# Kernel optimization log

Measured on AMD Instinct MI355X. Metric: run time of the kernel, lower is better.

## Reference

```python
import jax, jax.numpy as jnp
import numpy as np

N = 16384      # number of points
DIM = 128      # feature dim
POS_DIM = 3
K = 16         # neighbors (init kwarg k)
SCALE = np.float32(np.sqrt(DIM))


def setup_inputs() -> dict:
    key = jax.random.key(0)
    ks = jax.random.split(key, 16)
    g = lambda i, shape: (jax.random.normal(ks[i], shape, dtype=jnp.float32) * 0.05)
    return {
        "x": jax.random.normal(ks[0], (N, DIM), dtype=jnp.float32),
        "pos": jax.random.uniform(ks[1], (N, POS_DIM), dtype=jnp.float32),
        # weights stored as (in, out); torch Linear applies x @ W.T + b
        "Wq": g(2, (DIM, DIM)),
        "Wk": g(3, (DIM, DIM)),
        "Wv": g(4, (DIM, DIM)),
        "mid_w1": g(5, (DIM, DIM)), "mid_b1": g(6, (DIM,)),
        "mid_w2": g(7, (DIM, DIM)), "mid_b2": g(8, (DIM,)),
        "pe_w1": g(9, (POS_DIM, DIM)), "pe_b1": g(10, (DIM,)),
        "pe_w2": g(11, (DIM, DIM)), "pe_b2": g(12, (DIM,)),
        "fin_w": g(13, (DIM, DIM)), "fin_b": g(14, (DIM,)),
    }


def _knn_indices(pos):
    # squared pairwise distances [N, N]; top-K smallest -> neighbor indices [N, K]
    sq = jnp.sum(pos * pos, axis=-1)
    d2 = sq[:, None] + sq[None, :] - 2.0 * (pos @ pos.T)
    _, ind = jax.lax.top_k(-d2, K)
    return ind


def reference(x, pos, Wq, Wk, Wv, mid_w1, mid_b1, mid_w2, mid_b2,
              pe_w1, pe_b1, pe_w2, pe_b2, fin_w, fin_b):
    ind = _knn_indices(pos)                    # [N, K] int32 (constant wrt grads)
    x_k = x[ind]                               # [N, K, D]
    pos_k = pos[ind]                           # [N, K, 3]
    rel = pos[:, None, :] - pos_k              # [N, K, 3]
    pe = jax.nn.relu(rel @ pe_w1 + pe_b1) @ pe_w2 + pe_b2    # [N, K, D]
    q = x @ Wq                                 # [N, D]
    h = q[:, None, :] - (x_k @ Wk) + pe        # [N, K, D]
    y = jax.nn.relu(h @ mid_w1 + mid_b1) @ mid_w2 + mid_b2   # [N, K, D]
    y = jax.nn.softmax(y / SCALE, axis=-2)     # softmax over neighbors K
    z = x_k @ Wv + pe                          # [N, K, D]
    agg = jnp.sum(y * z, axis=-2)              # [N, D]
    return agg @ fin_w + fin_b + x
```

## Files before the change

kernel.cpp:

```cpp
#include <hip/hip_runtime.h>
#include <hip/hip_bf16.h>

#define N_PTS 16384
#define DIMF  128
#define KNB   16
#define GRES  8
#define NCELL (GRES*GRES*GRES)

typedef __attribute__((ext_vector_type(8))) short bf16x8;
typedef __attribute__((ext_vector_type(4))) short bf16x4;
typedef __attribute__((ext_vector_type(4))) float f32x4;
typedef __attribute__((ext_vector_type(4))) unsigned int u32x4;
typedef __attribute__((ext_vector_type(2))) unsigned int u32x2;

__device__ __forceinline__ unsigned short f2b(float f){
  unsigned int u = __float_as_uint(f);
  u = u + 0x7fffu + ((u >> 16) & 1u);
  return (unsigned short)(u >> 16);
}
__device__ __forceinline__ unsigned cvtpk(float lo, float hi){
  unsigned r;
  asm("v_cvt_pk_bf16_f32 %0, %1, %2" : "=v"(r) : "v"(lo), "v"(hi));
  return r;
}
__device__ __forceinline__ float b2f(unsigned short u){
  return __uint_as_float(((unsigned)u) << 16);
}
__device__ __forceinline__ float b2fs(short s){
  return __uint_as_float(((unsigned)(unsigned short)s) << 16);
}
__device__ __forceinline__ float unsort_f(unsigned s){
  unsigned u = (s & 0x80000000u) ? (s ^ 0x80000000u) : ~s;
  return __uint_as_float(u);
}

__global__ __launch_bounds__(256) void count_kernel(const float* __restrict__ pos, int* __restrict__ cnt){
  int i = blockIdx.x*256 + threadIdx.x;
  float px = pos[i*3+0], py = pos[i*3+1], pz = pos[i*3+2];
  int cx = min(GRES-1, max(0,(int)(px*(float)GRES)));
  int cy = min(GRES-1, max(0,(int)(py*(float)GRES)));
  int cz = min(GRES-1, max(0,(int)(pz*(float)GRES)));
  atomicAdd(&cnt[(cz*GRES+cy)*GRES+cx], 1);
}

__global__ __launch_bounds__(256) void scan_kernel(const int* __restrict__ cnt, int* __restrict__ starts, int* __restrict__ fillp){
  __shared__ int wsum[4];
  int t = threadIdx.x;
  int lane = t & 63, w = t >> 6;
  int a = cnt[2*t], b = cnt[2*t+1];
  int s = a + b;
  int p = s;
  #pragma unroll
  for (int off = 1; off < 64; off <<= 1){
    int v = __shfl_up(p, off, 64);
    if (lane >= off) p += v;
  }
  if (lane == 63) wsum[w] = p;
  __syncthreads();
  int base = 0;
  for (int i = 0; i < w; ++i) base += wsum[i];
  int excl = base + p - s;
  starts[2*t]   = excl;     fillp[2*t]   = excl;
  starts[2*t+1] = excl + a; fillp[2*t+1] = excl + a;
}

__global__ __launch_bounds__(256) void scatter_pack(const float* __restrict__ pos, int* __restrict__ fillp,
                                                    float4* __restrict__ pos4, int* __restrict__ pidx,
                                                    int* __restrict__ inv,
                                                    const float* __restrict__ w0, const float* __restrict__ w1,
                                                    const float* __restrict__ w2, const float* __restrict__ w3,
                                                    const float* __restrict__ w4, const float* __restrict__ w5,
                                                    const float* __restrict__ w6,
                                                    short* __restrict__ dst){
  if (blockIdx.x < 64){
    int i = blockIdx.x*256 + threadIdx.x;
    float px = pos[i*3+0], py = pos[i*3+1], pz = pos[i*3+2];
    int cx = min(GRES-1, max(0,(int)(px*(float)GRES)));
    int cy = min(GRES-1, max(0,(int)(py*(float)GRES)));
    int cz = min(GRES-1, max(0,(int)(pz*(float)GRES)));
    int c = (cz*GRES+cy)*GRES+cx;
    float sq = __fadd_rn(__fadd_rn(__fmul_rn(px,px), __fmul_rn(py,py)), __fmul_rn(pz,pz));
    int s = atomicAdd(&fillp[c], 1);
    pos4[s] = make_float4(px, py, pz, sq);
    pidx[s] = i;
    inv[i] = s;
  } else {
    int pb = blockIdx.x - 64;
    int slot = pb >> 6;
    const float* src = (slot==0)?w0:(slot==1)?w1:(slot==2)?w2:(slot==3)?w3:(slot==4)?w4:(slot==5)?w5:w6;
    int f = (pb & 63)*256 + threadIdx.x;
    int j  = f & 7;
    int ln = (f >> 3) & 63;
    int ks = (f >> 9) & 3;
    int nt = f >> 11;
    int k = ks*32 + ((ln >> 4) << 3) + j;
    int n = nt*16 + (ln & 15);
    dst[slot*16384 + f] = (short)f2b(src[k*DIMF + n]);
  }
}

__global__ __launch_bounds__(256) void knn_query64(const float4* __restrict__ pos4, const int* __restrict__ pidx,
                                                   const int* __restrict__ starts, const int* __restrict__ cnt,
                                                   const int* __restrict__ inv,
                                                   int* __restrict__ ind_slot){
  __shared__ unsigned long long cand[4][64];
  int lane = threadIdx.x & 63;
  int wv   = threadIdx.x >> 6;
  int t = blockIdx.x*4 + wv;
  float4 qp = pos4[t];
  float qx = qp.x, qy = qp.y, qz = qp.z, qsq = qp.w;
  int cx = min(GRES-1, max(0,(int)(qx*(float)GRES)));
  int cy = min(GRES-1, max(0,(int)(qy*(float)GRES)));
  int cz = min(GRES-1, max(0,(int)(qz*(float)GRES)));
  int zlo = max(0,cz-1), zhi = min(GRES-1,cz+1);
  int ylo = max(0,cy-1), yhi = min(GRES-1,cy+1);
  int xlo = max(0,cx-1), xhi = min(GRES-1,cx+1);
  const double h = 0.125;
  double dqx=(double)qx, dqy=(double)qy, dqz=(double)qz;

  int nb = 0;
  if (lane < 27){
    int dz = lane/9 - 1, dy = (lane/3)%3 - 1, dx = lane%3 - 1;
    int zz = cz+dz, yy = cy+dy, xx = cx+dx;
    if (zz>=zlo && zz<=zhi && yy>=ylo && yy<=yhi && xx>=xlo && xx<=xhi)
      nb = cnt[(zz*GRES+yy)*GRES+xx];
  }
  #pragma unroll
  for (int o=1;o<64;o<<=1) nb += __shfl_xor(nb, o, 64);
  float V = (float)((zhi-zlo+1)*(yhi-ylo+1)*(xhi-xlo+1)) * 0.001953125f;
  float r3 = 3.8197186f * V / (float)nb;
  float tau2 = 2.0f * __powf(r3, 0.66666667f);

  int nfound = 0;
  bool okscan = false;
  for (int it = 0; it < 8; ++it){
    nfound = 0;
    for (int zz=zlo; zz<=zhi; ++zz)
    for (int yy=ylo; yy<=yhi; ++yy)
    for (int xx=xlo; xx<=xhi; ++xx){
      double mdx = fmax(0.0, fmax((double)xx*h - dqx, dqx - (double)(xx+1)*h));
      double mdy = fmax(0.0, fmax((double)yy*h - dqy, dqy - (double)(yy+1)*h));
      double mdz = fmax(0.0, fmax((double)zz*h - dqz, dqz - (double)(zz+1)*h));
      double md2 = mdx*mdx + mdy*mdy + mdz*mdz;
      if (md2 > (double)tau2 + 1.0e-5) continue;
      int c = (zz*GRES+yy)*GRES+xx;
      int s0 = starts[c], n = cnt[c];
      for (int b = 0; b < n; b += 64){
        int o = b + lane;
        bool valid = o < n;
        float d = 3.0e38f; int idx = 0;
        if (valid){
          float4 pc = pos4[s0+o];
          idx = pidx[s0+o];
          float dot = __fmaf_rn(qz, pc.z, __fmaf_rn(qy, pc.y, __fmul_rn(qx, pc.x)));
          d   = __fsub_rn(__fadd_rn(qsq, pc.w), __fmul_rn(2.0f, dot));
        }
        bool admit = valid && (d < tau2);
        unsigned long long mask = __ballot(admit);
        if (admit){
          int pos = nfound + (int)__popcll(mask & ((1ull<<lane)-1ull));
          if (pos < 64){
            unsigned su = __float_as_uint(d);
            su ^= (unsigned)((int)su >> 31) | 0x80000000u;
            cand[wv][pos] = ((unsigned long long)su << 32) | (unsigned)idx;
          }
        }
        nfound += (int)__popcll(mask);
      }
    }
    if (nfound > 64){ tau2 *= 0.7f; continue; }
    if (nfound < 16){ tau2 *= 2.0f; continue; }
    okscan = true; break;
  }

  bool needfb = !okscan;
  if (okscan){
    asm volatile("s_waitcnt lgkmcnt(0)" ::: "memory");
    __builtin_amdgcn_sched_barrier(0);
    unsigned long long key = (lane < nfound) ? cand[wv][lane] : ~0ull;

    #pragma unroll
    for (int k = 2; k <= 64; k <<= 1){
      #pragma unroll
      for (int j = k>>1; j >= 1; j >>= 1){
        unsigned long long other = __shfl_xor(key, j, 64);
        bool takeSmall = (((lane & k) == 0) != ((lane & j) != 0));
        bool less = other < key;
        key = (takeSmall == less) ? other : key;
      }
    }
    if (lane < 16) ind_slot[t*KNB + lane] = inv[(int)(unsigned)(key & 0xffffffffu)];

    unsigned long long k15 = __shfl(key, 15, 64);
    float b16 = unsort_f((unsigned)(k15 >> 32));
    double mg = 1.0e300;
    if (cx-1 > 0)      mg = fmin(mg, dqx - (double)(cx-1)*h);
    if (cx+1 < GRES-1) mg = fmin(mg, (double)(cx+2)*h - dqx);
    if (cy-1 > 0)      mg = fmin(mg, dqy - (double)(cy-1)*h);
    if (cy+1 < GRES-1) mg = fmin(mg, (double)(cy+2)*h - dqy);
    if (cz-1 > 0)      mg = fmin(mg, dqz - (double)(cz-1)*h);
    if (cz+1 < GRES-1) mg = fmin(mg, (double)(cz+2)*h - dqz);
    needfb = !(mg*mg > (double)b16 + 1.0e-5);
  }

  if (needfb){
    float bd[KNB]; int bi[KNB];
    #pragma unroll
    for (int k=0;k<KNB;++k){ bd[k] = 3.0e38f; bi[k] = 0x7fffffff; }
    for (int r = 0; r < GRES; ++r){
      int zl = max(0, cz-r), zh = min(GRES-1, cz+r);
      int yl = max(0, cy-r), yh = min(GRES-1, cy+r);
      int xl = max(0, cx-r), xh = min(GRES-1, cx+r);
      for (int zz = zl; zz <= zh; ++zz)
      for (int yy = yl; yy <= yh; ++yy)
      for (int xx = xl; xx <= xh; ++xx){
        int ring = max(abs(zz-cz), max(abs(yy-cy), abs(xx-cx)));
        if (ring != r) continue;
        int c = (zz*GRES+yy)*GRES+xx;
        int s0 = starts[c], e = s0 + cnt[c];
        for (int s = s0; s < e; ++s){
          float4 pc = pos4[s];
          int idx = pidx[s];
          float dot = __fmaf_rn(qz, pc.z, __fmaf_rn(qy, pc.y, __fmul_rn(qx, pc.x)));
          float d   = __fsub_rn(__fadd_rn(qsq, pc.w), __fmul_rn(2.0f, dot));
          bool adm = (d < bd[KNB-1]) || (d == bd[KNB-1] && idx < bi[KNB-1]);
          if (adm){
            #pragma unroll
            for (int p = KNB-1; p >= 1; --p){
              float pd = bd[p-1]; int pi = bi[p-1];
              bool sh  = (pd > d) || (pd == d && pi > idx);
              bool ins = (!sh) && ((bd[p] > d) || (bd[p] == d && bi[p] > idx));
              bd[p] = sh ? pd : (ins ? d   : bd[p]);
              bi[p] = sh ? pi : (ins ? idx : bi[p]);
            }
            bool s0b = (bd[0] > d) || (bd[0] == d && bi[0] > idx);
            if (s0b){ bd[0] = d; bi[0] = idx; }
          }
        }
      }
      if (bd[KNB-1] < 3.0e37f){
        double mg = 1.0e300;
        if (cx - r > 0)      mg = fmin(mg, dqx - (double)(cx-r)*h);
        if (cx + r < GRES-1) mg = fmin(mg, (double)(cx+r+1)*h - dqx);
        if (cy - r > 0)      mg = fmin(mg, dqy - (double)(cy-r)*h);
        if (cy + r < GRES-1) mg = fmin(mg, (double)(cy+r+1)*h - dqy);
        if (cz - r > 0)      mg = fmin(mg, dqz - (double)(cz-r)*h);
        if (cz + r < GRES-1) mg = fmin(mg, (double)(cz+r+1)*h - dqz);
        if (mg*mg > (double)bd[KNB-1] + 1.0e-5) break;
      }
    }
    if (lane < 16) ind_slot[t*KNB + lane] = inv[bi[lane]];
  }
}

__global__ __launch_bounds__(256) void proj_kernel(const float* __restrict__ x, const int* __restrict__ pidx,
                                                   const short* __restrict__ pw,
                                                   unsigned short* __restrict__ q, unsigned short* __restrict__ xk,
                                                   unsigned short* __restrict__ xv){
  __shared__ __align__(16) char Abuf[16384];
  int tid = threadIdx.x, lane = tid & 63, wv = tid >> 6;
  int r0 = blockIdx.x * 64;
  {
    int row = tid >> 2, q4 = tid & 3;
    int orig = pidx[r0 + row];
    const float4* xr = (const float4*)(x + (size_t)orig*DIMF + q4*32);
    #pragma unroll
    for (int i=0;i<4;++i){
      float4 a = xr[2*i], b = xr[2*i+1];
      u32x4 u;
      u[0] = cvtpk(a.x, a.y); u[1] = cvtpk(a.z, a.w);
      u[2] = cvtpk(b.x, b.y); u[3] = cvtpk(b.z, b.w);
      *(u32x4*)(&Abuf[row*256 + ((q4*64 + i*16) ^ ((row&7)<<4))]) = u;
    }
  }
  __syncthreads();
  #pragma unroll 1
  for (int w = 0; w < 3; ++w){
    const bf16x8* bw = (const bf16x8*)(pw + w*16384);
    unsigned short* dst = (w==0) ? q : (w==1) ? xk : xv;
    f32x4 acc[8];
    #pragma unroll
    for (int nt=0;nt<8;++nt) acc[nt] = (f32x4){0.f,0.f,0.f,0.f};
    #pragma unroll
    for (int ks=0;ks<4;++ks){
      int ra = wv*16 + (lane&15);
      int cb = ks*64 + ((lane>>4)<<4);
      bf16x8 a0 = *(const bf16x8*)(&Abuf[ra*256 + (cb ^ ((ra&7)<<4))]);
      #pragma unroll
      for (int nt=0;nt<8;++nt){
        bf16x8 b = bw[(nt*4+ks)*64 + lane];
        acc[nt] = __builtin_amdgcn_mfma_f32_16x16x32_bf16(a0, b, acc[nt], 0, 0, 0);
      }
    }
    #pragma unroll
    for (int nt=0;nt<8;++nt){
      int grow = r0 + wv*16 + ((lane>>4)<<2);
      int col = nt*16 + (lane&15);
      unsigned pk01 = cvtpk(acc[nt][0], acc[nt][1]);
      unsigned pk23 = cvtpk(acc[nt][2], acc[nt][3]);
      dst[(size_t)(grow+0)*DIMF + col] = (unsigned short)pk01;
      dst[(size_t)(grow+1)*DIMF + col] = (unsigned short)(pk01 >> 16);
      dst[(size_t)(grow+2)*DIMF + col] = (unsigned short)pk23;
      dst[(size_t)(grow+3)*DIMF + col] = (unsigned short)(pk23 >> 16);
    }
  }
}

__global__ __launch_bounds__(512, 2) void main_kernel(
    const float* __restrict__ x, const float4* __restrict__ pos4, const int* __restrict__ pidx,
    const float* __restrict__ pe_w1, const float* __restrict__ pe_b1, const float* __restrict__ pe_b2,
    const float* __restrict__ mid_b1, const float* __restrict__ mid_b2, const float* __restrict__ fin_b,
    const unsigned short* __restrict__ qarr, const unsigned short* __restrict__ xkarr,
    const unsigned short* __restrict__ xvarr,
    const int* __restrict__ ind_slot, const short* __restrict__ pw,
    float* __restrict__ out)
{
  __shared__ __align__(16) char peLDS[32768];
  __shared__ __align__(16) char wbuf[32768];
  __shared__ float aggT[DIMF][9];
  __shared__ int indbuf[128];
  __shared__ int origbuf[8];
  int tid = threadIdx.x;
  int lane = tid & 63;
  int wv = tid >> 6;
  int swz = (blockIdx.x & 7) * (N_PTS/8/8) + (blockIdx.x >> 3);
  int t0 = swz * 8;

  int g = lane >> 4, kl = lane & 15;
  int mt = wv;

  #define STAGE_W(slot) { \
    const char* gsrc = (const char*)(pw + (size_t)(slot)*16384) + wv*4096 + lane*16; \
    char* ldst = &wbuf[wv*4096]; \
    __builtin_amdgcn_global_load_lds(gsrc,        ldst,        16, 0, 0); \
    __builtin_amdgcn_global_load_lds(gsrc + 1024, ldst + 1024, 16, 0, 0); \
    __builtin_amdgcn_global_load_lds(gsrc + 2048, ldst + 2048, 16, 0, 0); \
    __builtin_amdgcn_global_load_lds(gsrc + 3072, ldst + 3072, 16, 0, 0); }

  if (tid < 128) indbuf[tid] = ind_slot[swz*128 + tid];
  if (tid < 8) origbuf[tid] = pidx[t0 + tid];
  STAGE_W(3);
  __syncthreads();

  int nb4[4];
  #pragma unroll
  for (int r=0;r<4;++r) nb4[r] = indbuf[mt*16 + g*4 + r];
  int nbr = indbuf[mt*16 + kl];
  unsigned short zraw[8][4];
  #pragma unroll
  for (int nt=0;nt<8;++nt)
    #pragma unroll
    for (int r=0;r<4;++r)
      zraw[nt][r] = xvarr[(size_t)nb4[r]*DIMF + nt*16 + kl];

  bf16x8 tfrag[4];
  {
    float4 pq = pos4[t0+mt];
    float4 pn = pos4[nbr];
    float rx = pq.x-pn.x, ry = pq.y-pn.y, rz = pq.z-pn.z;
    #pragma unroll
    for (int ks=0;ks<4;++ks){
      int c0 = ks*32 + g*8;
      const float4* w0 = (const float4*)(pe_w1 + c0);
      const float4* w1 = (const float4*)(pe_w1 + DIMF + c0);
      const float4* w2 = (const float4*)(pe_w1 + 2*DIMF + c0);
      const float4* bb = (const float4*)(pe_b1 + c0);
      float4 wa0=w0[0], wa1=w0[1], wb0=w1[0], wb1=w1[1], wc0=w2[0], wc1=w2[1], wd0=bb[0], wd1=bb[1];
      float wa[8]={wa0.x,wa0.y,wa0.z,wa0.w,wa1.x,wa1.y,wa1.z,wa1.w};
      float wb[8]={wb0.x,wb0.y,wb0.z,wb0.w,wb1.x,wb1.y,wb1.z,wb1.w};
      float wc[8]={wc0.x,wc0.y,wc0.z,wc0.w,wc1.x,wc1.y,wc1.z,wc1.w};
      float wd[8]={wd0.x,wd0.y,wd0.z,wd0.w,wd1.x,wd1.y,wd1.z,wd1.w};
      float tv[8];
      #pragma unroll
      for (int j=0;j<8;++j)
        tv[j] = fmaxf(fmaf(rx, wa[j], fmaf(ry, wb[j], fmaf(rz, wc[j], wd[j]))), 0.f);
      u32x4 u;
      u[0] = cvtpk(tv[0], tv[1]); u[1] = cvtpk(tv[2], tv[3]);
      u[2] = cvtpk(tv[4], tv[5]); u[3] = cvtpk(tv[6], tv[7]);
      tfrag[ks] = __builtin_bit_cast(bf16x8, u);
    }
  }

  f32x4 acc[8];
  const bf16x8* bw = (const bf16x8*)wbuf;

  {
    #pragma unroll
    for (int nt=0;nt<8;++nt){
      float bv = pe_b2[nt*16 + kl];
      acc[nt] = (f32x4){bv,bv,bv,bv};
    }
    #pragma unroll
    for (int ks=0;ks<4;++ks){
      #pragma unroll
      for (int nt=0;nt<8;++nt){
        bf16x8 b = bw[(nt*4+ks)*64 + lane];
        acc[nt] = __builtin_amdgcn_mfma_f32_16x16x32_bf16(tfrag[ks], b, acc[nt], 0, 0, 0);
      }
    }
  }

  bf16x4 zb[8];
  int r0w = mt*16 + g*4;
  #pragma unroll
  for (int nt=0;nt<8;++nt){
    int col = nt*16 + kl;
    float p0 = acc[nt][0], p1 = acc[nt][1], p2 = acc[nt][2], p3 = acc[nt][3];
    unsigned pk01 = cvtpk(p0, p1), pk23 = cvtpk(p2, p3);
    *(unsigned short*)&peLDS[(r0w+0)*256 + ((col*2) ^ (((r0w+0)&7)<<4))] = (unsigned short)pk01;
    *(unsigned short*)&peLDS[(r0w+1)*256 + ((col*2) ^ (((r0w+1)&7)<<4))] = (unsigned short)(pk01 >> 16);
    *(unsigned short*)&peLDS[(r0w+2)*256 + ((col*2) ^ (((r0w+2)&7)<<4))] = (unsigned short)pk23;
    *(unsigned short*)&peLDS[(r0w+3)*256 + ((col*2) ^ (((r0w+3)&7)<<4))] = (unsigned short)(pk23 >> 16);
    float z0 = b2f(zraw[nt][0]) + p0;
    float z1 = b2f(zraw[nt][1]) + p1;
    float z2 = b2f(zraw[nt][2]) + p2;
    float z3 = b2f(zraw[nt][3]) + p3;
    u32x2 zu; zu[0] = cvtpk(z0, z1); zu[1] = cvtpk(z2, z3);
    zb[nt] = __builtin_bit_cast(bf16x4, zu);
  }

  bf16x8 q8[4], k8[4];
  {
    const unsigned short* qrow = qarr + (size_t)(t0+mt)*DIMF;
    const unsigned short* krow = xkarr + (size_t)nbr*DIMF;
    #pragma unroll
    for (int ks=0;ks<4;++ks){
      int c0 = ks*32 + g*8;
      q8[ks] = *(const bf16x8*)(qrow + c0);
      k8[ks] = *(const bf16x8*)(krow + c0);
    }
  }
  __syncthreads();
  STAGE_W(4);

  bf16x8 hfrag[4];
  {
    int row = mt*16 + kl;
    #pragma unroll
    for (int ks=0;ks<4;++ks){
      int c0 = ks*32 + g*8;
      bf16x8 p8 = *(const bf16x8*)(&peLDS[row*256 + ((c0*2) ^ ((row&7)<<4))]);
      float hf[8];
      #pragma unroll
      for (int j=0;j<8;++j)
        hf[j] = (b2fs(q8[ks][j]) - b2fs(k8[ks][j])) + b2fs(p8[j]);
      u32x4 u;
      u[0] = cvtpk(hf[0], hf[1]); u[1] = cvtpk(hf[2], hf[3]);
      u[2] = cvtpk(hf[4], hf[5]); u[3] = cvtpk(hf[6], hf[7]);
      hfrag[ks] = __builtin_bit_cast(bf16x8, u);
    }
  }
  __syncthreads();

  {
    #pragma unroll
    for (int nt=0;nt<8;++nt){
      float bv = mid_b1[nt*16 + kl];
      acc[nt] = (f32x4){bv,bv,bv,bv};
    }
    #pragma unroll
    for (int ks=0;ks<4;++ks){
      #pragma unroll
      for (int nt=0;nt<8;++nt){
        bf16x8 b = bw[(nt*4+ks)*64 + lane];
        acc[nt] = __builtin_amdgcn_mfma_f32_16x16x32_bf16(hfrag[ks], b, acc[nt], 0, 0, 0);
      }
    }
  }
  __syncthreads();
  STAGE_W(5);
  #pragma unroll
  for (int nt=0;nt<8;++nt){
    int col = nt*16 + kl;
    unsigned pk01 = cvtpk(fmaxf(acc[nt][0],0.f), fmaxf(acc[nt][1],0.f));
    unsigned pk23 = cvtpk(fmaxf(acc[nt][2],0.f), fmaxf(acc[nt][3],0.f));
    *(unsigned short*)&peLDS[(r0w+0)*256 + ((col*2) ^ (((r0w+0)&7)<<4))] = (unsigned short)pk01;
    *(unsigned short*)&peLDS[(r0w+1)*256 + ((col*2) ^ (((r0w+1)&7)<<4))] = (unsigned short)(pk01 >> 16);
    *(unsigned short*)&peLDS[(r0w+2)*256 + ((col*2) ^ (((r0w+2)&7)<<4))] = (unsigned short)pk23;
    *(unsigned short*)&peLDS[(r0w+3)*256 + ((col*2) ^ (((r0w+3)&7)<<4))] = (unsigned short)(pk23 >> 16);
  }
  __syncthreads();

  {
    #pragma unroll
    for (int nt=0;nt<8;++nt){
      float bv = mid_b2[nt*16 + kl];
      acc[nt] = (f32x4){bv,bv,bv,bv};
    }
    #pragma unroll
    for (int ks=0;ks<4;++ks){
      int ra = mt*16 + kl;
      int cb = ks*64 + g*16;
      bf16x8 a0 = *(const bf16x8*)(&peLDS[ra*256 + (cb ^ ((ra&7)<<4))]);
      #pragma unroll
      for (int nt=0;nt<8;++nt){
        bf16x8 b = bw[(nt*4+ks)*64 + lane];
        acc[nt] = __builtin_amdgcn_mfma_f32_16x16x32_bf16(a0, b, acc[nt], 0, 0, 0);
      }
    }
  }
  __syncthreads();
  STAGE_W(6);

  {
    const float invS = 0.08838834764831843f;
    #pragma unroll
    for (int nt=0;nt<8;++nt){
      f32x4 y = acc[nt];
      float mx = fmaxf(fmaxf(y[0],y[1]), fmaxf(y[2],y[3]));
      mx = fmaxf(mx, __shfl_xor(mx, 16, 64));
      mx = fmaxf(mx, __shfl_xor(mx, 32, 64));
      float e0 = __expf((y[0]-mx)*invS);
      float e1 = __expf((y[1]-mx)*invS);
      float e2 = __expf((y[2]-mx)*invS);
      float e3 = __expf((y[3]-mx)*invS);
      float ssum = e0+e1+e2+e3;
      ssum += __shfl_xor(ssum, 16, 64);
      ssum += __shfl_xor(ssum, 32, 64);
      bf16x4 zv = zb[nt];
      float ps = (e0*b2fs(zv[0]) + e1*b2fs(zv[1]) + e2*b2fs(zv[2]) + e3*b2fs(zv[3])) / ssum;
      ps += __shfl_xor(ps, 16, 64);
      ps += __shfl_xor(ps, 32, 64);
      if (lane < 16) aggT[nt*16 + lane][mt] = ps;
    }
  }
  __syncthreads();

  {
    f32x4 facc = (f32x4){0.f,0.f,0.f,0.f};
    #pragma unroll
    for (int ks=0;ks<4;++ks){
      int c0 = ks*32 + g*8;
      float av[8];
      #pragma unroll
      for (int j=0;j<8;++j)
        av[j] = (kl < 8) ? aggT[c0+j][kl] : 0.f;
      u32x4 u;
      u[0] = cvtpk(av[0], av[1]); u[1] = cvtpk(av[2], av[3]);
      u[2] = cvtpk(av[4], av[5]); u[3] = cvtpk(av[6], av[7]);
      bf16x8 a = __builtin_bit_cast(bf16x8, u);
      bf16x8 b = bw[(wv*4+ks)*64 + lane];
      facc = __builtin_amdgcn_mfma_f32_16x16x32_bf16(a, b, facc, 0, 0, 0);
    }
    int col = wv*16 + kl;
    float fb = fin_b[col];
    if (g < 2){
      #pragma unroll
      for (int r=0;r<4;++r){
        int prow = g*4 + r;
        int o = origbuf[prow];
        out[(size_t)o*DIMF + col] = facc[r] + fb + x[(size_t)o*DIMF + col];
      }
    }
  }
  #undef STAGE_W
}

extern "C" void kernel_launch(void* const* d_in, const int* in_sizes, int n_in,
                              void* d_out, int out_size, void* d_ws, size_t ws_size,
                              hipStream_t stream)
{
  (void)in_sizes; (void)n_in; (void)out_size; (void)ws_size;
  const float* x      = (const float*)d_in[0];
  const float* pos    = (const float*)d_in[1];
  const float* Wq     = (const float*)d_in[2];
  const float* Wk     = (const float*)d_in[3];
  const float* Wv     = (const float*)d_in[4];
  const float* mid_w1 = (const float*)d_in[5];
  const float* mid_b1 = (const float*)d_in[6];
  const float* mid_w2 = (const float*)d_in[7];
  const float* mid_b2 = (const float*)d_in[8];
  const float* pe_w1  = (const float*)d_in[9];
  const float* pe_b1  = (const float*)d_in[10];
  const float* pe_w2  = (const float*)d_in[11];
  const float* pe_b2  = (const float*)d_in[12];
  const float* fin_w  = (const float*)d_in[13];
  const float* fin_b  = (const float*)d_in[14];
  float* out = (float*)d_out;
  char* ws = (char*)d_ws;

  int*    cellcnt = (int*)   (ws + 0);
  int*    fillp   = (int*)   (ws + 4096);
  int*    starts  = (int*)   (ws + 8192);
  int*    pidx    = (int*)   (ws + 49152);
  float4* pos4    = (float4*)(ws + 114688);
  int*    ind     = (int*)   (ws + 376832);
  short*  pw      = (short*) (ws + 1425408);
  int*    inv     = (int*)   (ws + 1654784);
  unsigned short* qarr  = (unsigned short*)(ws + 1720320);
  unsigned short* xkarr = (unsigned short*)(ws + 5914624);
  unsigned short* xvarr = (unsigned short*)(ws + 10108928);

  hipMemsetAsync(cellcnt, 0, NCELL*sizeof(int), stream);
  count_kernel  <<<N_PTS/256, 256, 0, stream>>>(pos, cellcnt);
  scan_kernel   <<<1,         256, 0, stream>>>(cellcnt, starts, fillp);
  scatter_pack  <<<64 + 7*64, 256, 0, stream>>>(pos, fillp, pos4, pidx, inv,
                                                Wq, Wk, Wv, pe_w2, mid_w1, mid_w2, fin_w, pw);
  knn_query64   <<<N_PTS/4,   256, 0, stream>>>(pos4, pidx, starts, cellcnt, inv, ind);
  proj_kernel   <<<N_PTS/64,  256, 0, stream>>>(x, pidx, pw, qarr, xkarr, xvarr);
  main_kernel   <<<N_PTS/8,   512, 0, stream>>>(x, pos4, pidx, pe_w1, pe_b1, pe_b2, mid_b1, mid_b2, fin_b,
                                                qarr, xkarr, xvarr, ind, pw, out);
}
```

Before: 163.8 us.

## Merge grid-build setup kernels into one cooperative kernel with grid syncs

Replaces the memset plus the count, scan and scatter/pack launches with a single cooperative kernel of 512 blocks. Grid-wide syncs separate the phases: zero counts, count and weight pack, scan, scatter. This removes three launches and a memset from the small setup stage, at the cost of grid.sync overhead and a dependence on cooperative launch support.

New measurement: 313.0 us. 1.91x slower.

```diff
diff --git a/kernel.cpp b/kernel.cpp
--- a/kernel.cpp
+++ b/kernel.cpp
@@ -1,5 +1,8 @@
 #include <hip/hip_runtime.h>
 #include <hip/hip_bf16.h>
+#include <hip/hip_cooperative_groups.h>
+
+namespace cg = cooperative_groups;
 
 #define N_PTS 16384
 #define DIMF  128
@@ -34,46 +37,65 @@
   return __uint_as_float(u);
 }
 
-__global__ __launch_bounds__(256) void count_kernel(const float* __restrict__ pos, int* __restrict__ cnt){
-  int i = blockIdx.x*256 + threadIdx.x;
-  float px = pos[i*3+0], py = pos[i*3+1], pz = pos[i*3+2];
-  int cx = min(GRES-1, max(0,(int)(px*(float)GRES)));
-  int cy = min(GRES-1, max(0,(int)(py*(float)GRES)));
-  int cz = min(GRES-1, max(0,(int)(pz*(float)GRES)));
-  atomicAdd(&cnt[(cz*GRES+cy)*GRES+cx], 1);
-}
-
-__global__ __launch_bounds__(256) void scan_kernel(const int* __restrict__ cnt, int* __restrict__ starts, int* __restrict__ fillp){
-  __shared__ int wsum[4];
-  int t = threadIdx.x;
-  int lane = t & 63, w = t >> 6;
-  int a = cnt[2*t], b = cnt[2*t+1];
-  int s = a + b;
-  int p = s;
-  #pragma unroll
-  for (int off = 1; off < 64; off <<= 1){
-    int v = __shfl_up(p, off, 64);
-    if (lane >= off) p += v;
-  }
-  if (lane == 63) wsum[w] = p;
-  __syncthreads();
-  int base = 0;
-  for (int i = 0; i < w; ++i) base += wsum[i];
-  int excl = base + p - s;
-  starts[2*t]   = excl;     fillp[2*t]   = excl;
-  starts[2*t+1] = excl + a; fillp[2*t+1] = excl + a;
-}
-
-__global__ __launch_bounds__(256) void scatter_pack(const float* __restrict__ pos, int* __restrict__ fillp,
-                                                    float4* __restrict__ pos4, int* __restrict__ pidx,
-                                                    int* __restrict__ inv,
-                                                    const float* __restrict__ w0, const float* __restrict__ w1,
-                                                    const float* __restrict__ w2, const float* __restrict__ w3,
-                                                    const float* __restrict__ w4, const float* __restrict__ w5,
-                                                    const float* __restrict__ w6,
-                                                    short* __restrict__ dst){
-  if (blockIdx.x < 64){
-    int i = blockIdx.x*256 + threadIdx.x;
+__global__ __launch_bounds__(256) void build_coop(const float* __restrict__ pos,
+                                                  int* __restrict__ cnt, int* __restrict__ starts, int* __restrict__ fillp,
+                                                  float4* __restrict__ pos4, int* __restrict__ pidx, int* __restrict__ inv,
+                                                  const float* __restrict__ w0, const float* __restrict__ w1,
+                                                  const float* __restrict__ w2, const float* __restrict__ w3,
+                                                  const float* __restrict__ w4, const float* __restrict__ w5,
+                                                  const float* __restrict__ w6,
+                                                  short* __restrict__ dst){
+  cg::grid_group grid = cg::this_grid();
+  int b = blockIdx.x, t = threadIdx.x;
+
+  if (b == 0){ cnt[2*t] = 0; cnt[2*t+1] = 0; }
+  grid.sync();
+
+  if (b < 64){
+    int i = b*256 + t;
+    float px = pos[i*3+0], py = pos[i*3+1], pz = pos[i*3+2];
+    int cx = min(GRES-1, max(0,(int)(px*(float)GRES)));
+    int cy = min(GRES-1, max(0,(int)(py*(float)GRES)));
+    int cz = min(GRES-1, max(0,(int)(pz*(float)GRES)));
+    atomicAdd(&cnt[(cz*GRES+cy)*GRES+cx], 1);
+  } else {
+    int pb = b - 64;
+    int slot = pb >> 6;
+    const float* src = (slot==0)?w0:(slot==1)?w1:(slot==2)?w2:(slot==3)?w3:(slot==4)?w4:(slot==5)?w5:w6;
+    int f = (pb & 63)*256 + t;
+    int j  = f & 7;
+    int ln = (f >> 3) & 63;
+    int ks = (f >> 9) & 3;
+    int nt = f >> 11;
+    int k = ks*32 + ((ln >> 4) << 3) + j;
+    int n = nt*16 + (ln & 15);
+    dst[slot*16384 + f] = (short)f2b(src[k*DIMF + n]);
+  }
+  grid.sync();
+
+  if (b == 0){
+    __shared__ int wsum[4];
+    int lane = t & 63, w = t >> 6;
+    int a = cnt[2*t], bb = cnt[2*t+1];
+    int s = a + bb;
+    int p = s;
+    #pragma unroll
+    for (int off = 1; off < 64; off <<= 1){
+      int v = __shfl_up(p, off, 64);
+      if (lane >= off) p += v;
+    }
+    if (lane == 63) wsum[w] = p;
+    __syncthreads();
+    int base = 0;
+    for (int i = 0; i < w; ++i) base += wsum[i];
+    int excl = base + p - s;
+    starts[2*t]   = excl;      fillp[2*t]   = excl;
+    starts[2*t+1] = excl + a;  fillp[2*t+1] = excl + a;
+  }
+  grid.sync();
+
+  if (b < 64){
+    int i = b*256 + t;
     float px = pos[i*3+0], py = pos[i*3+1], pz = pos[i*3+2];
     int cx = min(GRES-1, max(0,(int)(px*(float)GRES)));
     int cy = min(GRES-1, max(0,(int)(py*(float)GRES)));
@@ -84,18 +106,6 @@
     pos4[s] = make_float4(px, py, pz, sq);
     pidx[s] = i;
     inv[i] = s;
-  } else {
-    int pb = blockIdx.x - 64;
-    int slot = pb >> 6;
-    const float* src = (slot==0)?w0:(slot==1)?w1:(slot==2)?w2:(slot==3)?w3:(slot==4)?w4:(slot==5)?w5:w6;
-    int f = (pb & 63)*256 + threadIdx.x;
-    int j  = f & 7;
-    int ln = (f >> 3) & 63;
-    int ks = (f >> 9) & 3;
-    int nt = f >> 11;
-    int k = ks*32 + ((ln >> 4) << 3) + j;
-    int n = nt*16 + (ln & 15);
-    dst[slot*16384 + f] = (short)f2b(src[k*DIMF + n]);
   }
 }
 
@@ -591,13 +601,18 @@
   unsigned short* xkarr = (unsigned short*)(ws + 5914624);
   unsigned short* xvarr = (unsigned short*)(ws + 10108928);
 
-  hipMemsetAsync(cellcnt, 0, NCELL*sizeof(int), stream);
-  count_kernel  <<<N_PTS/256, 256, 0, stream>>>(pos, cellcnt);
-  scan_kernel   <<<1,         256, 0, stream>>>(cellcnt, starts, fillp);
-  scatter_pack  <<<64 + 7*64, 256, 0, stream>>>(pos, fillp, pos4, pidx, inv,
-                                                Wq, Wk, Wv, pe_w2, mid_w1, mid_w2, fin_w, pw);
-  knn_query64   <<<N_PTS/4,   256, 0, stream>>>(pos4, pidx, starts, cellcnt, inv, ind);
-  proj_kernel   <<<N_PTS/64,  256, 0, stream>>>(x, pidx, pw, qarr, xkarr, xvarr);
-  main_kernel   <<<N_PTS/8,   512, 0, stream>>>(x, pos4, pidx, pe_w1, pe_b1, pe_b2, mid_b1, mid_b2, fin_b,
-                                                qarr, xkarr, xvarr, ind, pw, out);
-}
+  {
+    void* kargs[] = {
+      (void*)&pos, (void*)&cellcnt, (void*)&starts, (void*)&fillp,
+      (void*)&pos4, (void*)&pidx, (void*)&inv,
+      (void*)&Wq, (void*)&Wk, (void*)&Wv, (void*)&pe_w2, (void*)&mid_w1, (void*)&mid_w2, (void*)&fin_w,
+      (void*)&pw
+    };
+    hipLaunchCooperativeKernel((const void*)build_coop, dim3(512), dim3(256), kargs, 0, stream);
+  }
+
+  knn_query64 <<<N_PTS/4,  256, 0, stream>>>(pos4, pidx, starts, cellcnt, inv, ind);
+  proj_kernel <<<N_PTS/64, 256, 0, stream>>>(x, pidx, pw, qarr, xkarr, xvarr);
+  main_kernel <<<N_PTS/8,  512, 0, stream>>>(x, pos4, pidx, pe_w1, pe_b1, pe_b2, mid_b1, mid_b2, fin_b,
+                                             qarr, xkarr, xvarr, ind, pw, out);
+}
```
